# Kernel optimization log

Measured on AMD Instinct MI355X. Metric: run time of the kernel, lower is better.

## Reference

```python
import jax, jax.numpy as jnp
import numpy as np


def _normalize_xyz_with_pc(pc, xyz):
    # Center by point-cloud centroid, scale by max radius of centered cloud.
    center = pc.mean(axis=1, keepdims=True)                      # [B,1,3]
    pc_c = pc - center
    scale = jnp.sqrt((pc_c ** 2).sum(-1)).max(axis=1)            # [B]
    scale = jnp.maximum(scale, 1e-6)[:, None, None]              # [B,1,1]
    return (xyz - center) / scale


def _nn_gather(seed_n, pts_n, feat):
    # seed_n [B,M,3], pts_n [B,K,3], feat [B,C,K] -> [B,C,M]
    d2 = ((seed_n ** 2).sum(-1)[:, :, None]
          + (pts_n ** 2).sum(-1)[:, None, :]
          - 2.0 * jnp.einsum('bmd,bkd->bmk', seed_n, pts_n))     # [B,M,K]
    idx = jnp.argmin(d2, axis=-1)                                # [B,M]
    return jnp.take_along_axis(feat, idx[:, None, :], axis=2)    # [B,C,M]


def _conv1x1(w, b, x):
    # w [O,C], b [O], x [B,C,M] -> [B,O,M]
    return jnp.einsum('oc,bcm->bom', w, x) + b[None, :, None]


def setup_inputs() -> dict:
    key = jax.random.key(0)
    ks = jax.random.split(key, 10)
    B, N, M, K, D = 4, 20000, 1024, 16384, 768
    return {
        'point_cloud': jax.random.normal(ks[0], (B, N, 3), jnp.float32),
        'seed_xyz': jax.random.normal(ks[1], (B, M, 3), jnp.float32),
        'seed_features': jax.random.normal(ks[2], (B, 256, M), jnp.float32),
        'pts': jax.random.normal(ks[3], (B, K, 3), jnp.float32),
        'feat': jax.random.normal(ks[4], (B, D, K), jnp.float32),
        'ln_gamma': jnp.ones((D,), jnp.float32),
        'ln_beta': jnp.zeros((D,), jnp.float32),
        'pw1': jax.random.normal(ks[5], (256, D), jnp.float32) * 0.02,
        'pb1': jnp.zeros((256,), jnp.float32),
        'pw2': jax.random.normal(ks[6], (256, 256), jnp.float32) * 0.02,
        'pb2': jnp.zeros((256,), jnp.float32),
        'fw1': jax.random.normal(ks[7], (256, 512), jnp.float32) * 0.02,
        'fb1': jnp.zeros((256,), jnp.float32),
        'fw2': jax.random.normal(ks[8], (256, 256), jnp.float32) * 0.02,
        'fb2': jnp.zeros((256,), jnp.float32),
    }


def reference(point_cloud, seed_xyz, seed_features, pts, feat,
              ln_gamma, ln_beta, pw1, pb1, pw2, pb2, fw1, fb1, fw2, fb2):
    seed_n = _normalize_xyz_with_pc(point_cloud, seed_xyz)       # [B,M,3]
    pts_n = _normalize_xyz_with_pc(point_cloud, pts)             # [B,K,3]
    vggt_raw = _nn_gather(seed_n, pts_n, feat)                   # [B,768,M]

    # LayerNorm over channel dim (applied on [B,M,768] in the original)
    x = vggt_raw.transpose(0, 2, 1)                              # [B,M,768]
    mu = x.mean(-1, keepdims=True)
    var = x.var(-1, keepdims=True)
    x_ln = ((x - mu) * jax.lax.rsqrt(var + 1e-5) * ln_gamma + ln_beta)
    x_ln = x_ln.transpose(0, 2, 1)                               # [B,768,M]

    vggt_proj = _conv1x1(pw2, pb2, jax.nn.relu(_conv1x1(pw1, pb1, x_ln)))
    fused = jnp.concatenate([seed_features, vggt_proj], axis=1)  # [B,512,M]
    mixed = _conv1x1(fw2, fb2, jax.nn.relu(_conv1x1(fw1, fb1, fused)))
    return mixed                                                 # [B,256,M]
```

## Files before the change

kernel.cpp:

```cpp
#include <hip/hip_runtime.h>
#include <math.h>

#define B_ 4
#define N_ 20000
#define M_ 1024
#define K_ 16384
#define D_ 768

typedef __attribute__((ext_vector_type(8))) short bf16x8;
typedef __attribute__((ext_vector_type(4))) float f32x4;

#define OFF_PART   0ul
#define OFF_RAD    1024ul
#define OFF_IDX    4096ul
#define OFF_G      2097152ul
#define OFF_XLN    16777216ul
#define OFF_FUSED  25165824ul
#define OFF_H2     29360128ul
#define OFF_WB1    33554432ul
#define OFF_WCAT   34603008ul
#define OFF_WB4    35651584ul
#define OFF_BC     36700160ul

__device__ inline unsigned short f2bf(float x) {
    union { float f; unsigned int u; } v; v.f = x;
    unsigned int r = v.u + 0x7fffu + ((v.u >> 16) & 1u);
    return (unsigned short)(r >> 16);
}

__device__ inline void gload_lds16(const void* g, void* lds) {
    __builtin_amdgcn_global_load_lds(
        (const __attribute__((address_space(1))) unsigned int*)g,
        (__attribute__((address_space(3))) unsigned int*)lds, 16, 0, 0);
}

__device__ inline void reduce_center(const float* part, int b,
                                     float& cx, float& cy, float& cz)
{
    cx = 0.f; cy = 0.f; cz = 0.f;
    #pragma unroll
    for (int r = 0; r < 16; ++r) {
        cx += part[(b*16+r)*3+0];
        cy += part[(b*16+r)*3+1];
        cz += part[(b*16+r)*3+2];
    }
    cx *= (1.f/N_); cy *= (1.f/N_); cz *= (1.f/N_);
}

__device__ inline float reduce_scale(const float* rad, int b)
{
    float m = 0.f;
    #pragma unroll
    for (int r = 0; r < 16; ++r) m = fmaxf(m, rad[b*16+r]);
    return fmaxf(sqrtf(m), 1e-6f);
}

__global__ __launch_bounds__(256) void k_pre(
    const float* __restrict__ pc,
    const float* __restrict__ pw1, const float* __restrict__ pw2,
    const float* __restrict__ pb2,
    const float* __restrict__ fw1, const float* __restrict__ fb1,
    const float* __restrict__ fw2,
    unsigned short* __restrict__ Wb1, unsigned short* __restrict__ Wcat,
    unsigned short* __restrict__ Wb4, float* __restrict__ bc,
    float* __restrict__ part)
{
    int bid = blockIdx.x, t = threadIdx.x;
    int lane = t & 63, wv = t >> 6;
    __shared__ float red[3][4];

    if (bid < 768) {
        int i0 = bid*256 + t;
        Wb1[i0] = f2bf(pw1[i0]);
        if (i0 < 65536) {
            int o = i0 >> 8, c = i0 & 255;
            Wcat[(size_t)o*512 + c] = f2bf(fw1[(size_t)o*512 + c]);
            Wb4[i0] = f2bf(fw2[i0]);
        }
    }
    if (bid < 256) {
        const float* fb = fw1 + (size_t)bid*512 + 256;
        float acc = 0.f;
        for (int j = 0; j < 256; ++j)
            acc = fmaf(fb[j], pw2[j*256 + t], acc);
        Wcat[(size_t)bid*512 + 256 + t] = f2bf(acc);
        float v = fb[t] * pb2[t];
        for (int off = 32; off; off >>= 1) v += __shfl_down(v, off, 64);
        if (!lane) red[0][wv] = v;
        __syncthreads();
        if (!t) bc[bid] = red[0][0]+red[0][1]+red[0][2]+red[0][3] + fb1[bid];
    } else if (bid >= 768) {
        int pi = bid - 768;
        int b = pi >> 4, chunk = pi & 15;
        const float* p = pc + (size_t)b * N_ * 3;
        int i0 = chunk * 1250;
        float sx = 0.f, sy = 0.f, sz = 0.f;
        for (int i = i0 + t; i < i0 + 1250; i += 256) {
            sx += p[i*3+0]; sy += p[i*3+1]; sz += p[i*3+2];
        }
        for (int off = 32; off; off >>= 1) {
            sx += __shfl_down(sx, off, 64);
            sy += __shfl_down(sy, off, 64);
            sz += __shfl_down(sz, off, 64);
        }
        if (!lane) { red[0][wv] = sx; red[1][wv] = sy; red[2][wv] = sz; }
        __syncthreads();
        if (!t) {
            part[(b*16+chunk)*3+0] = red[0][0]+red[0][1]+red[0][2]+red[0][3];
            part[(b*16+chunk)*3+1] = red[1][0]+red[1][1]+red[1][2]+red[1][3];
            part[(b*16+chunk)*3+2] = red[2][0]+red[2][1]+red[2][2]+red[2][3];
        }
    }
}

__global__ __launch_bounds__(256) void k_cs_rad(const float* __restrict__ pc,
                                                const float* __restrict__ part,
                                                float* __restrict__ rad)
{
    int blk = blockIdx.x, b = blk >> 4, pi = blk & 15;
    float cx, cy, cz;
    reduce_center(part, b, cx, cy, cz);
    const float* p = pc + (size_t)b * N_ * 3;
    int tid = threadIdx.x;
    int i0 = pi * 1250;
    float mx = 0.f;
    for (int i = i0 + tid; i < i0 + 1250; i += 256) {
        float dx = p[i*3+0]-cx, dy = p[i*3+1]-cy, dz = p[i*3+2]-cz;
        mx = fmaxf(mx, dx*dx + dy*dy + dz*dz);
    }
    for (int off = 32; off; off >>= 1) mx = fmaxf(mx, __shfl_down(mx, off, 64));
    __shared__ float red[4];
    int w = tid >> 6, l = tid & 63;
    if (!l) red[w] = mx;
    __syncthreads();
    if (!tid) rad[b*16+pi] = fmaxf(fmaxf(red[0], red[1]), fmaxf(red[2], red[3]));
}

__global__ __launch_bounds__(256) void k_nn(const float* __restrict__ seed_xyz,
                                            const float* __restrict__ pts,
                                            const float* __restrict__ part,
                                            const float* __restrict__ rad,
                                            int* __restrict__ idx)
{
    int blk = blockIdx.x, b = blk >> 7, g = blk & 127;
    float cx, cy, cz;
    reduce_center(part, b, cx, cy, cz);
    float scinv = 1.f / reduce_scale(rad, b);
    int t = threadIdx.x;
    int j = t & 31, s = t >> 5;
    int m = g*8 + s;
    const float* sp = seed_xyz + ((size_t)b*M_ + m)*3;
    float sx = (sp[0]-cx)*scinv, sy = (sp[1]-cy)*scinv, sz = (sp[2]-cz)*scinv;
    float ssq = sx*sx + sy*sy + sz*sz;
    const float* pb = pts + (size_t)b*K_*3;

    float best[4] = {3.4e38f, 3.4e38f, 3.4e38f, 3.4e38f};
    int   bk[4]   = {0, 0, 0, 0};
    for (int i = 0; i < 512; i += 4) {
        #pragma unroll
        for (int r = 0; r < 4; ++r) {
            int k = (i + r)*32 + j;
            const float* pp = pb + (size_t)k*3;
            float px = (pp[0]-cx)*scinv, py = (pp[1]-cy)*scinv, pz = (pp[2]-cz)*scinv;
            float qw = px*px + py*py + pz*pz;
            float d2 = ssq + qw - 2.f*(sx*px + sy*py + sz*pz);
            if (d2 < best[r]) { best[r] = d2; bk[r] = k; }
        }
    }
    float bm = best[0]; int bmk = bk[0];
    #pragma unroll
    for (int r = 1; r < 4; ++r) {
        if (best[r] < bm || (best[r] == bm && bk[r] < bmk)) { bm = best[r]; bmk = bk[r]; }
    }
    #pragma unroll
    for (int mask = 16; mask; mask >>= 1) {
        float ob = __shfl_xor(bm, mask, 64);
        int   ok = __shfl_xor(bmk, mask, 64);
        if (ob < bm || (ob == bm && ok < bmk)) { bm = ob; bmk = ok; }
    }
    if (j == 0) idx[b*M_ + m] = bmk;
}

__global__ __launch_bounds__(256) void k_gather_tsf(const float* __restrict__ feat,
                                                    const int* __restrict__ idx,
                                                    const float* __restrict__ sf,
                                                    float* __restrict__ G,
                                                    unsigned short* __restrict__ fused)
{
    int bid = blockIdx.x, t = threadIdx.x;
    if (bid < 3072) {
        int b = bid / 768, c = bid - b*768;
        const float* frow = feat + ((size_t)b*D_ + c) * K_;
        const int* ib = idx + b*M_;
        float* grow = G + ((size_t)b*D_ + c) * M_;
        #pragma unroll
        for (int r = 0; r < 4; ++r) {
            int m = r*256 + t;
            grow[m] = frow[ib[m]];
        }
    } else {
        __shared__ float tile[32][33];
        int id = bid - 3072;
        int b = id >> 8, rem = id & 255;
        int m0 = (rem & 31) * 32, c0 = (rem >> 5) * 32;
        int tx = t & 31, ty = t >> 5;
        #pragma unroll
        for (int rr = 0; rr < 32; rr += 8)
            tile[ty+rr][tx] = sf[((size_t)b*256 + c0+ty+rr)*M_ + m0 + tx];
        __syncthreads();
        #pragma unroll
        for (int rr = 0; rr < 32; rr += 8)
            fused[((size_t)(b*M_ + m0+ty+rr))*512 + c0 + tx] = f2bf(tile[tx][ty+rr]);
    }
}

__global__ __launch_bounds__(256) void k_ln_fused(const float* __restrict__ G,
                                                  const float* __restrict__ gamma,
                                                  const float* __restrict__ beta,
                                                  unsigned short* __restrict__ xln)
{
    int b = blockIdx.y, m0 = blockIdx.x * 32;
    int t = threadIdx.x;
    int ml = t & 31, cp = t >> 5;
    const float* Gb = G + (size_t)b * D_ * M_;
    float s = 0.f, q = 0.f;
    for (int c = cp; c < D_; c += 8) {
        float v = Gb[(size_t)c*M_ + m0 + ml];
        s += v; q += v*v;
    }
    __shared__ float sred[8][32], qred[8][32];
    __shared__ float mu[32], iv[32];
    sred[cp][ml] = s; qred[cp][ml] = q;
    __syncthreads();
    if (t < 32) {
        float S = 0.f, Q = 0.f;
        #pragma unroll
        for (int r = 0; r < 8; ++r) { S += sred[r][t]; Q += qred[r][t]; }
        float m_ = S * (1.f/768.f);
        mu[t] = m_;
        iv[t] = rsqrtf(Q * (1.f/768.f) - m_*m_ + 1e-5f);
    }
    __syncthreads();

    __shared__ float tile[64][33];
    int ty = t >> 5;
    int cx2 = t & 31;
    for (int c0 = 0; c0 < D_; c0 += 64) {
        __syncthreads();
        #pragma unroll
        for (int ri = 0; ri < 8; ++ri) {
            int cl = ty*8 + ri;
            tile[cl][ml] = Gb[(size_t)(c0+cl)*M_ + m0 + ml];
        }
        __syncthreads();
        float2 ga = *(const float2*)&gamma[c0 + 2*cx2];
        float2 be = *(const float2*)&beta[c0 + 2*cx2];
        #pragma unroll
        for (int ri = 0; ri < 4; ++ri) {
            int m_l = ty*4 + ri;
            float v0 = (tile[2*cx2+0][m_l] - mu[m_l]) * iv[m_l] * ga.x + be.x;
            float v1 = (tile[2*cx2+1][m_l] - mu[m_l]) * iv[m_l] * ga.y + be.y;
            ushort2 pk = make_ushort2(f2bf(v0), f2bf(v1));
            *(ushort2*)&xln[((size_t)((b<<10) + m0 + m_l))*D_ + c0 + 2*cx2] = pk;
        }
    }
}

__global__ __launch_bounds__(256) void k_gemm_mfma(
    const unsigned short* __restrict__ X, const unsigned short* __restrict__ W,
    const float* __restrict__ bias, int Kdim, int relu, int mode,
    unsigned short* __restrict__ Ybf, int rowStride, int colOff,
    float* __restrict__ Yf)
{
    __shared__ unsigned short Al[64*64];
    __shared__ unsigned short Wl[64*64];
    int t = threadIdx.x, l = t & 63, w = t >> 6;
    int m0 = blockIdx.x * 64, o0 = blockIdx.y * 64;
    f32x4 acc[4];
    #pragma unroll
    for (int j = 0; j < 4; ++j) acc[j] = (f32x4){0.f, 0.f, 0.f, 0.f};

    for (int kc = 0; kc < Kdim; kc += 64) {
        #pragma unroll
        for (int i = 0; i < 2; ++i) {
            int lin = i*4096 + w*1024;
            int lb  = lin + l*16;
            int row = lb >> 7;
            int k16 = (lb >> 4) & 7;
            int ks  = k16 ^ (row & 7);
            gload_lds16(X + (size_t)(m0+row)*Kdim + kc + ks*8, (char*)Al + lin);
            gload_lds16(W + (size_t)(o0+row)*Kdim + kc + ks*8, (char*)Wl + lin);
        }
        __syncthreads();
        #pragma unroll
        for (int kk = 0; kk < 2; ++kk) {
            int arow = w*16 + (l & 15);
            int h = l >> 4;
            bf16x8 a = *(const bf16x8*)&Al[arow*64 + (((kk<<2)|h) ^ (arow & 7))*8];
            #pragma unroll
            for (int j = 0; j < 4; ++j) {
                int orow = j*16 + (l & 15);
                bf16x8 bfr = *(const bf16x8*)&Wl[orow*64 + (((kk<<2)|h) ^ (orow & 7))*8];
                acc[j] = __builtin_amdgcn_mfma_f32_16x16x32_bf16(a, bfr, acc[j], 0, 0, 0);
            }
        }
        __syncthreads();
    }

    int mbase = m0 + w*16 + (l >> 4)*4;
    if (mode == 0) {
        #pragma unroll
        for (int j = 0; j < 4; ++j) {
            int o = o0 + j*16 + (l & 15);
            float bi = bias[o];
            #pragma unroll
            for (int r = 0; r < 4; ++r) {
                float v = acc[j][r] + bi;
                if (relu) v = fmaxf(v, 0.f);
                Ybf[(size_t)(mbase + r)*rowStride + colOff + o] = f2bf(v);
            }
        }
    } else {
        int b = mbase >> 10, ml = mbase & 1023;
        #pragma unroll
        for (int j = 0; j < 4; ++j) {
            int o = o0 + j*16 + (l & 15);
            float bi = bias[o];
            float4 sv = make_float4(acc[j][0]+bi, acc[j][1]+bi, acc[j][2]+bi, acc[j][3]+bi);
            *(float4*)&Yf[((size_t)(b*256 + o))*1024 + ml] = sv;
        }
    }
}

extern "C" void kernel_launch(void* const* d_in, const int* in_sizes, int n_in,
                              void* d_out, int out_size, void* d_ws, size_t ws_size,
                              hipStream_t stream)
{
    (void)in_sizes; (void)n_in; (void)out_size; (void)ws_size;
    const float* pc        = (const float*)d_in[0];
    const float* seed_xyz  = (const float*)d_in[1];
    const float* seed_feat = (const float*)d_in[2];
    const float* pts       = (const float*)d_in[3];
    const float* feat      = (const float*)d_in[4];
    const float* ln_g      = (const float*)d_in[5];
    const float* ln_b      = (const float*)d_in[6];
    const float* pw1       = (const float*)d_in[7];
    const float* pb1       = (const float*)d_in[8];
    const float* pw2       = (const float*)d_in[9];
    const float* pb2       = (const float*)d_in[10];
    const float* fw1       = (const float*)d_in[11];
    const float* fb1       = (const float*)d_in[12];
    const float* fw2       = (const float*)d_in[13];
    const float* fb2       = (const float*)d_in[14];
    float* out = (float*)d_out;

    char* ws = (char*)d_ws;
    float*          part  = (float*)(ws + OFF_PART);
    float*          rad   = (float*)(ws + OFF_RAD);
    int*            idx   = (int*)(ws + OFF_IDX);
    float*          G     = (float*)(ws + OFF_G);
    unsigned short* xln   = (unsigned short*)(ws + OFF_XLN);
    unsigned short* fused = (unsigned short*)(ws + OFF_FUSED);
    unsigned short* h2    = (unsigned short*)(ws + OFF_H2);
    unsigned short* Wb1   = (unsigned short*)(ws + OFF_WB1);
    unsigned short* Wcat  = (unsigned short*)(ws + OFF_WCAT);
    unsigned short* Wb4   = (unsigned short*)(ws + OFF_WB4);
    float*          bc    = (float*)(ws + OFF_BC);

    k_pre<<<832, 256, 0, stream>>>(pc, pw1, pw2, pb2, fw1, fb1, fw2,
                                   Wb1, Wcat, Wb4, bc, part);
    k_cs_rad<<<64, 256, 0, stream>>>(pc, part, rad);
    k_nn<<<512, 256, 0, stream>>>(seed_xyz, pts, part, rad, idx);
    k_gather_tsf<<<4096, 256, 0, stream>>>(feat, idx, seed_feat, G, fused);
    k_ln_fused<<<dim3(M_/32, B_), 256, 0, stream>>>(G, ln_g, ln_b, xln);
    k_gemm_mfma<<<dim3(64, 4), 256, 0, stream>>>(xln, Wb1, pb1, 768, 1, 0, fused, 512, 256, nullptr);
    k_gemm_mfma<<<dim3(64, 4), 256, 0, stream>>>(fused, Wcat, bc, 512, 1, 0, h2, 256, 0, nullptr);
    k_gemm_mfma<<<dim3(64, 4), 256, 0, stream>>>(h2, Wb4, fb2, 256, 0, 1, nullptr, 0, 0, out);
}
```

Measured before the change: 163.7 us.

## Precompute normalized points and split nearest-neighbor search over K into partial reductions

Adds a prep kernel that normalizes pts once into float4 (xyz plus squared norm), so the NN search no longer redoes normalization per seed and reads a single 16-byte vector per point. The NN search is split into four K-chunks across 2048 blocks instead of 512, which raises occupancy on a GPU with many CUs, and a small reduce kernel then merges the partial argmins with lowest-index tie-breaking. The cost is two extra kernel launches and a small workspace round trip.

```diff
diff --git a/kernel.cpp b/kernel.cpp
--- a/kernel.cpp
+++ b/kernel.cpp
@@ -13,6 +13,8 @@
 #define OFF_PART   0ul
 #define OFF_RAD    1024ul
 #define OFF_IDX    4096ul
+#define OFF_P4     32768ul
+#define OFF_NNP    1179648ul
 #define OFF_G      2097152ul
 #define OFF_XLN    16777216ul
 #define OFF_FUSED  25165824ul
@@ -136,13 +138,29 @@
     if (!tid) rad[b*16+pi] = fmaxf(fmaxf(red[0], red[1]), fmaxf(red[2], red[3]));
 }
 
-__global__ __launch_bounds__(256) void k_nn(const float* __restrict__ seed_xyz,
-                                            const float* __restrict__ pts,
-                                            const float* __restrict__ part,
-                                            const float* __restrict__ rad,
-                                            int* __restrict__ idx)
-{
-    int blk = blockIdx.x, b = blk >> 7, g = blk & 127;
+__global__ __launch_bounds__(256) void k_prep_pts(const float* __restrict__ pts,
+                                                  const float* __restrict__ part,
+                                                  const float* __restrict__ rad,
+                                                  float4* __restrict__ P4)
+{
+    int blk = blockIdx.x, b = blk >> 6;
+    float cx, cy, cz;
+    reduce_center(part, b, cx, cy, cz);
+    float sc = 1.f / reduce_scale(rad, b);
+    int k = (blk & 63)*256 + threadIdx.x;
+    const float* pp = pts + ((size_t)b*K_ + k)*3;
+    float px = (pp[0]-cx)*sc, py = (pp[1]-cy)*sc, pz = (pp[2]-cz)*sc;
+    P4[(size_t)b*K_ + k] = make_float4(px, py, pz, px*px + py*py + pz*pz);
+}
+
+__global__ __launch_bounds__(256) void k_nn_part(const float* __restrict__ seed_xyz,
+                                                 const float4* __restrict__ P4,
+                                                 const float* __restrict__ part,
+                                                 const float* __restrict__ rad,
+                                                 float2* __restrict__ nnp)
+{
+    int blk = blockIdx.x;
+    int ks = blk & 3, g = (blk >> 2) & 127, b = blk >> 9;
     float cx, cy, cz;
     reduce_center(part, b, cx, cy, cz);
     float scinv = 1.f / reduce_scale(rad, b);
@@ -152,33 +170,46 @@
     const float* sp = seed_xyz + ((size_t)b*M_ + m)*3;
     float sx = (sp[0]-cx)*scinv, sy = (sp[1]-cy)*scinv, sz = (sp[2]-cz)*scinv;
     float ssq = sx*sx + sy*sy + sz*sz;
-    const float* pb = pts + (size_t)b*K_*3;
+    const float4* Pb = P4 + (size_t)b*K_ + ks*4096;
 
     float best[4] = {3.4e38f, 3.4e38f, 3.4e38f, 3.4e38f};
     int   bk[4]   = {0, 0, 0, 0};
-    for (int i = 0; i < 512; i += 4) {
+    for (int i = 0; i < 128; i += 4) {
         #pragma unroll
         for (int r = 0; r < 4; ++r) {
-            int k = (i + r)*32 + j;
-            const float* pp = pb + (size_t)k*3;
-            float px = (pp[0]-cx)*scinv, py = (pp[1]-cy)*scinv, pz = (pp[2]-cz)*scinv;
-            float qw = px*px + py*py + pz*pz;
-            float d2 = ssq + qw - 2.f*(sx*px + sy*py + sz*pz);
-            if (d2 < best[r]) { best[r] = d2; bk[r] = k; }
+            int kk = (i + r)*32 + j;
+            float4 q = Pb[kk];
+            float d2 = ssq + q.w - 2.f*(sx*q.x + sy*q.y + sz*q.z);
+            if (d2 < best[r]) { best[r] = d2; bk[r] = kk; }
         }
     }
     float bm = best[0]; int bmk = bk[0];
     #pragma unroll
-    for (int r = 1; r < 4; ++r) {
+    for (int r = 1; r < 4; ++r)
         if (best[r] < bm || (best[r] == bm && bk[r] < bmk)) { bm = best[r]; bmk = bk[r]; }
-    }
     #pragma unroll
     for (int mask = 16; mask; mask >>= 1) {
         float ob = __shfl_xor(bm, mask, 64);
         int   ok = __shfl_xor(bmk, mask, 64);
         if (ob < bm || (ob == bm && ok < bmk)) { bm = ob; bmk = ok; }
     }
-    if (j == 0) idx[b*M_ + m] = bmk;
+    if (j == 0)
+        nnp[((size_t)(b*M_ + m) << 2) + ks] = make_float2(bm, __int_as_float(ks*4096 + bmk));
+}
+
+__global__ __launch_bounds__(256) void k_nn_reduce(const float2* __restrict__ nnp,
+                                                   int* __restrict__ idx)
+{
+    int i = blockIdx.x*256 + threadIdx.x;
+    float bm = 3.4e38f; int bmk = 0;
+    bool first = true;
+    #pragma unroll
+    for (int r = 0; r < 4; ++r) {
+        float2 v = nnp[((size_t)i << 2) + r];
+        int k = __float_as_int(v.y);
+        if (first || v.x < bm || (v.x == bm && k < bmk)) { bm = v.x; bmk = k; first = false; }
+    }
+    idx[i] = bmk;
 }
 
 __global__ __launch_bounds__(256) void k_gather_tsf(const float* __restrict__ feat,
@@ -358,6 +389,8 @@
     float*          part  = (float*)(ws + OFF_PART);
     float*          rad   = (float*)(ws + OFF_RAD);
     int*            idx   = (int*)(ws + OFF_IDX);
+    float4*         P4    = (float4*)(ws + OFF_P4);
+    float2*         nnp   = (float2*)(ws + OFF_NNP);
     float*          G     = (float*)(ws + OFF_G);
     unsigned short* xln   = (unsigned short*)(ws + OFF_XLN);
     unsigned short* fused = (unsigned short*)(ws + OFF_FUSED);
@@ -370,7 +403,9 @@
     k_pre<<<832, 256, 0, stream>>>(pc, pw1, pw2, pb2, fw1, fb1, fw2,
                                    Wb1, Wcat, Wb4, bc, part);
     k_cs_rad<<<64, 256, 0, stream>>>(pc, part, rad);
-    k_nn<<<512, 256, 0, stream>>>(seed_xyz, pts, part, rad, idx);
+    k_prep_pts<<<256, 256, 0, stream>>>(pts, part, rad, P4);
+    k_nn_part<<<2048, 256, 0, stream>>>(seed_xyz, P4, part, rad, nnp);
+    k_nn_reduce<<<16, 256, 0, stream>>>(nnp, idx);
     k_gather_tsf<<<4096, 256, 0, stream>>>(feat, idx, seed_feat, G, fused);
     k_ln_fused<<<dim3(M_/32, B_), 256, 0, stream>>>(G, ln_g, ln_b, xln);
     k_gemm_mfma<<<dim3(64, 4), 256, 0, stream>>>(xln, Wb1, pb1, 768, 1, 0, fused, 512, 256, nullptr);
```

Result: faster. 147.9 us (-9.6%).
